# Kernel optimization log

Measured on AMD Instinct MI355X. Metric: run time of the kernel, lower is better.

## Reference

```python
import jax, jax.numpy as jnp
import numpy as np
from jax import lax

B, T, I, H = 128, 48, 128, 512


def setup_inputs() -> dict:
    key = jax.random.key(0)
    ks = jax.random.split(key, 16)
    s = lambda *sh: 1.0 / np.sqrt(sh[-1])
    inp = {
        "decoder_x": jax.random.normal(ks[0], (B, T, I), jnp.float32),
        "x": jax.random.normal(ks[1], (B, T, 3), jnp.float32),
        # xavier_normal for [num_layers=1, B, H] -> std = sqrt(2/(B+H))
        "h0": jax.random.normal(ks[2], (B, H), jnp.float32) * np.sqrt(2.0 / (B + H)),
        "W1": jax.random.normal(ks[3], (H, H), jnp.float32) * s(H),
        "b1": jnp.zeros((H,), jnp.float32),
        "W2": jax.random.normal(ks[4], (H, I), jnp.float32) * s(I),
        "b2": jnp.zeros((H,), jnp.float32),
        "W3": jax.random.normal(ks[5], (1, H), jnp.float32) * s(H),
        "b3": jnp.zeros((1,), jnp.float32),
        "W4": jax.random.normal(ks[6], (H, I + 3), jnp.float32) * s(I + 3),
        "b4": jnp.zeros((H,), jnp.float32),
        "W_ih": jax.random.normal(ks[7], (3 * H, H), jnp.float32) * s(H),
        "W_hh": jax.random.normal(ks[8], (3 * H, H), jnp.float32) * s(H),
        "b_ih": jnp.zeros((3 * H,), jnp.float32),
        "b_hh": jnp.zeros((3 * H,), jnp.float32),
        "Wfc": jax.random.normal(ks[9], (1, H), jnp.float32) * s(H),
        "bfc": jnp.zeros((1,), jnp.float32),
    }
    return inp


def reference(decoder_x, x, h0, W1, b1, W2, b2, W3, b3, W4, b4,
              W_ih, W_hh, b_ih, b_hh, Wfc, bfc):
    Bc, Tc, Ic = decoder_x.shape
    # layer2(decoder_x) is step-invariant: compute once. [B, T, H]
    w2 = jnp.einsum('bti,hi->bth', decoder_x, W2) + b2

    def step(carry, x_t):
        h, _ = carry  # h: [B, H]
        w1 = h @ W1.T + b1                              # [B, H]
        # attention energies over the T_1 encoder window
        e = jnp.tanh(w1[:, None, :] + w2) @ W3[0] + b3[0]   # [B, T]
        a = jax.nn.softmax(e, axis=1)                   # [B, T]
        c = jnp.einsum('bti,bt->bi', decoder_x, a)      # weighted context [B, I]
        y0 = jnp.concatenate([c, x_t], axis=1) @ W4.T + b4  # [B, H]
        # single-step GRU (PyTorch gate order r, z, n)
        gi = y0 @ W_ih.T + b_ih
        gh = h @ W_hh.T + b_hh
        ir, iz, in_ = jnp.split(gi, 3, axis=1)
        hr, hz, hn = jnp.split(gh, 3, axis=1)
        r = jax.nn.sigmoid(ir + hr)
        z = jax.nn.sigmoid(iz + hz)
        n = jnp.tanh(in_ + r * hn)
        h_new = (1.0 - z) * n + z * h
        return (h_new, a), None

    xs = jnp.swapaxes(x, 0, 1)  # [T, B, 3]
    (h_f, a_f), _ = lax.scan(step, (h0, jnp.zeros((Bc, Tc), decoder_x.dtype)), xs)
    re = h_f @ Wfc.T + bfc      # fc(final_output[:, -1, :])  -> [B, 1]
    return re, a_f[:, :, None]  # weighted_alpha from last step [B, T, 1]
```

## Files before the change

kernel.cpp:

```cpp
#include <hip/hip_runtime.h>


typedef _Float16 half8 __attribute__((ext_vector_type(8)));
typedef _Float16 h2v  __attribute__((ext_vector_type(2)));
typedef float    f32x4 __attribute__((ext_vector_type(4)));
typedef unsigned int u32x3 __attribute__((ext_vector_type(3)));

#define OFF_BAR   0u
#define OFF_BZ    32768u
#define OFF_BC    40960u
#define OFF_WZ    65536u
#define OFF_WCT   2162688u
#define OFF_W2H   3178496u
#define OFF_HGH   9732096u
#define OFF_ZG    9863168u
#define OFF_DW    10911744u

__device__ __forceinline__ float fexp2(float x) { return __builtin_amdgcn_exp2f(x); }
__device__ __forceinline__ float frcp(float x)  { return __builtin_amdgcn_rcpf(x); }
__device__ __forceinline__ float fast_tanh(float x) {
  x = fminf(fmaxf(x, -15.f), 15.f);
  float e = fexp2(x * 2.8853900817779268f);
  return (e - 1.f) * frcp(e + 1.f);
}
__device__ __forceinline__ float fast_sigmoid(float x) {
  x = fminf(fmaxf(x, -30.f), 30.f);
  float e = fexp2(x * 1.4426950408889634f);
  return e * frcp(e + 1.f);
}

__device__ __forceinline__ void st_f32(float* p, float v) {
  __hip_atomic_store(p, v, __ATOMIC_RELAXED, __HIP_MEMORY_SCOPE_AGENT);
}
__device__ __forceinline__ unsigned long long ld_u64(const void* p) {
  return __hip_atomic_load((const unsigned long long*)p, __ATOMIC_RELAXED,
                           __HIP_MEMORY_SCOPE_AGENT);
}
__device__ __forceinline__ void st_u32(unsigned int* p, unsigned int v) {
  __hip_atomic_store(p, v, __ATOMIC_RELAXED, __HIP_MEMORY_SCOPE_AGENT);
}
union U2 { unsigned long long u; float f[2]; };
union H4 { unsigned long long u; _Float16 h[4]; };
union HU { unsigned int u; h2v h; };

__device__ __forceinline__ void poll_ge(unsigned int* fp, bool active,
                                        unsigned int target) {
  for (;;) {
    unsigned int v = active
      ? __hip_atomic_load(fp, __ATOMIC_RELAXED, __HIP_MEMORY_SCOPE_AGENT)
      : target;
    if (__ballot(v < target) == 0) break;
    __builtin_amdgcn_s_sleep(1);
  }
  __asm__ __volatile__("" ::: "memory");
}

__global__ __launch_bounds__(256) void prep_all(
    const float* __restrict__ dx, const float* __restrict__ h0,
    const float* __restrict__ W1, const float* __restrict__ Whh,
    const float* __restrict__ b1, const float* __restrict__ bhh,
    const float* __restrict__ Wih, const float* __restrict__ W4,
    const float* __restrict__ b4, const float* __restrict__ bih,
    const float* __restrict__ W2, const float* __restrict__ b2,
    _Float16* __restrict__ hgh,
    _Float16* __restrict__ Wzh, float* __restrict__ bz,
    float* __restrict__ bc, _Float16* __restrict__ WcT,
    _Float16* __restrict__ w2h, unsigned int* __restrict__ bar)
{
  __shared__ __align__(16) char smem[58368];
  const int bid = blockIdx.x;
  const int tid = threadIdx.x;
  const int lane = tid & 63, wv = tid >> 6;

  if (bid == 0) {
    for (int i = tid; i < 8192; i += 256) bar[i] = 0u;
  } else if (bid == 1) {
    for (int n = tid; n < 2048; n += 256)
      bz[n] = (n < 512) ? b1[n] : bhh[n - 512];
  } else if (bid < 18) {
    const int o0 = (bid - 2) * 96 + wv * 24;
    for (int it = 0; it < 24; ++it) {
      const int row = o0 + it;
      const float* r = Wih + row * 512 + lane * 8;
      float s = 0.f;
#pragma unroll
      for (int u = 0; u < 8; ++u) s += r[u] * b4[lane * 8 + u];
#pragma unroll
      for (int off = 32; off >= 1; off >>= 1) s += __shfl_xor(s, off);
      if (lane == 0) bc[row] = bih[row] + s;
    }
  } else if (bid < 34) {
    const int i0 = (bid - 18) * 4096 + tid * 16;
#pragma unroll
    for (int u = 0; u < 4; ++u) {
      float4 v = *(const float4*)(h0 + i0 + u * 4);
      H4 p; p.h[0] = (_Float16)v.x; p.h[1] = (_Float16)v.y;
      p.h[2] = (_Float16)v.z; p.h[3] = (_Float16)v.w;
      *(unsigned long long*)(hgh + i0 + u * 4) = p.u;
    }
  } else if (bid < 98) {
    const int i0 = (bid - 34) * 16384 + tid * 64;
#pragma unroll 4
    for (int u = 0; u < 16; ++u) {
      const int i = i0 + u * 4;
      const float* src = (i < 262144) ? (W1 + i) : (Whh + i - 262144);
      float4 v = *(const float4*)src;
      H4 p; p.h[0] = (_Float16)v.x; p.h[1] = (_Float16)v.y;
      p.h[2] = (_Float16)v.z; p.h[3] = (_Float16)v.w;
      *(unsigned long long*)(Wzh + i) = p.u;
    }
  } else if (bid < 194) {
    float* wih = (float*)smem;
    float* w4s = (float*)(smem + 4224);
    const int o0 = (bid - 98) * 16;
    const int k = tid;
    float acc[16];
#pragma unroll
    for (int i = 0; i < 16; ++i) acc[i] = 0.f;
    for (int jc = 0; jc < 512; jc += 64) {
      __syncthreads();
      for (int idx = tid; idx < 16 * 64; idx += 256) {
        int oo = idx >> 6, jj = idx & 63;
        wih[oo * 66 + jj] = Wih[(o0 + oo) * 512 + jc + jj];
      }
      for (int idx = tid; idx < 64 * 131; idx += 256) {
        int r = idx / 131, c = idx - r * 131;
        w4s[r * 132 + c] = W4[(jc + r) * 131 + c];
      }
      __syncthreads();
      if (k < 131) {
        for (int jj = 0; jj < 64; ++jj) {
          float w4v = w4s[jj * 132 + k];
#pragma unroll
          for (int oo = 0; oo < 16; ++oo) acc[oo] += wih[oo * 66 + jj] * w4v;
        }
      }
    }
    if (k < 131) {
#pragma unroll
      for (int oo = 0; oo < 16; ++oo)
        WcT[k * 1536 + o0 + oo] = (_Float16)acc[oo];
    }
  } else {
    float* dxa = (float*)smem;
    _Float16* w2t = (_Float16*)(smem + 24576);
    const int b = bid - 194;
    for (int idx = tid; idx < 48 * 128; idx += 256)
      dxa[idx] = dx[b * 6144 + idx];
    for (int hc = 0; hc < 4; ++hc) {
      __syncthreads();
      for (int idx = tid; idx < 128 * 128; idx += 256) {
        int hl = idx >> 7, i = idx & 127;
        w2t[i * 132 + hl] = (_Float16)W2[(hc * 128 + hl) * 128 + i];
      }
      __syncthreads();
      const int hh = tid & 127;
      const int tq = tid >> 7;
      const float b2v = b2[hc * 128 + hh];
      for (int tt = tq * 24; tt < tq * 24 + 24; ++tt) {
        float acc = b2v;
#pragma unroll 4
        for (int i = 0; i < 128; ++i)
          acc += dxa[tt * 128 + i] * (float)w2t[i * 132 + hh];
        w2h[(b * 48 + tt) * 512 + hc * 128 + hh] = (_Float16)acc;
      }
    }
  }
}

__global__ __launch_bounds__(256) void prep_dw(
    const float* __restrict__ dx, const _Float16* __restrict__ WcT,
    unsigned int* __restrict__ DW12)
{
  __shared__ float dxu[16 * 128];
  const int j = blockIdx.x;
  const int tid = threadIdx.x;
  const int u0 = j * 16;
  const float4* src = (const float4*)(dx + (size_t)u0 * 128);
  float4* dst4 = (float4*)dxu;
  for (int i = tid; i < 512; i += 256) dst4[i] = src[i];
  __syncthreads();
  const int c0 = tid * 2;
  float acc[16][6];
#pragma unroll
  for (int u = 0; u < 16; ++u)
#pragma unroll
    for (int g = 0; g < 6; ++g) acc[u][g] = 0.f;
  for (int k = 0; k < 128; ++k) {
    const _Float16* wr = WcT + k * 1536 + c0;
    h2v w0 = *(const h2v*)(wr);
    h2v w1v = *(const h2v*)(wr + 512);
    h2v w2v = *(const h2v*)(wr + 1024);
    const float f0 = (float)w0[0],  f1 = (float)w0[1];
    const float f2 = (float)w1v[0], f3 = (float)w1v[1];
    const float f4 = (float)w2v[0], f5 = (float)w2v[1];
#pragma unroll
    for (int u = 0; u < 16; ++u) {
      const float d = dxu[u * 128 + k];
      acc[u][0] += d * f0; acc[u][1] += d * f1; acc[u][2] += d * f2;
      acc[u][3] += d * f3; acc[u][4] += d * f4; acc[u][5] += d * f5;
    }
  }
#pragma unroll
  for (int u = 0; u < 16; ++u) {
    unsigned int* o = DW12 + (size_t)(u0 + u) * 768 + tid * 3;
    HU p;
    p.h[0] = (_Float16)acc[u][0]; p.h[1] = (_Float16)acc[u][1]; o[0] = p.u;
    p.h[0] = (_Float16)acc[u][2]; p.h[1] = (_Float16)acc[u][3]; o[1] = p.u;
    p.h[0] = (_Float16)acc[u][4]; p.h[1] = (_Float16)acc[u][5]; o[2] = p.u;
  }
}

#define DW_STEP(TB, CUR)                                                     \
  do {                                                                       \
    _Pragma("unroll")                                                        \
    for (int j = 0; j < 4; ++j) {                                            \
      const float a = asx[(TB) * 4 + j];                                     \
      HU p0, p1, p2; p0.u = CUR[j].x; p1.u = CUR[j].y; p2.u = CUR[j].z;      \
      aR0 += a * (float)p0.h[0]; aR1 += a * (float)p0.h[1];                  \
      aZ0 += a * (float)p1.h[0]; aZ1 += a * (float)p1.h[1];                  \
      aN0 += a * (float)p2.h[0]; aN1 += a * (float)p2.h[1];                  \
    }                                                                        \
    if ((TB) < 9) {                                                          \
      _Pragma("unroll")                                                      \
      for (int j = 0; j < 4; ++j)                                            \
        CUR[j] = *(const u32x3*)(dwp + (size_t)(((TB) + 3) * 4 + j) * 768);  \
    }                                                                        \
  } while (0)

__global__ __launch_bounds__(512, 2) void decoder_main(
    const float* __restrict__ xin, const float* __restrict__ h0,
    const float* __restrict__ W3, const float* __restrict__ b3,
    const float* __restrict__ Wfc, const float* __restrict__ bfc,
    const _Float16* __restrict__ Wzh, const float* __restrict__ bz,
    const _Float16* __restrict__ WcT, const float* __restrict__ bc,
    const _Float16* __restrict__ w2h, const unsigned int* __restrict__ DW12,
    _Float16* __restrict__ hgh, float* __restrict__ zg,
    unsigned int* __restrict__ bar, float* __restrict__ out)
{
  const int tid  = threadIdx.x;
  const int lane = tid & 63;
  const int wv   = tid >> 6;
  const int bid  = blockIdx.x;
  const int grp  = bid & 7;
  const int mem  = bid >> 3;
  const int b0   = grp * 16;
  const int myrow = b0 + mem;
  const int cb   = mem * 128;
  const int myIdx = grp * 16 + mem;
  const int base16 = grp * 16;
  unsigned int* zflag = bar;
  unsigned int* hflag = bar + 4096;

  __shared__ __align__(16) _Float16 w2lds[48 * 512];
  __shared__ __align__(16) char hlds[16384];
  __shared__ __align__(16) unsigned int dwlds[24 * 768];
  __shared__ float xlds[48 * 4];
  __shared__ float wfcs[512];
  __shared__ float es[48];
  __shared__ float asx[48];
  __shared__ float red[4];

  const int m = lane & 15, q = lane >> 4;

  half8 wzf[16];
  const int ncol = cb + wv * 16 + m;
  {
    const _Float16* wrow = Wzh + ncol * 512 + q * 8;
#pragma unroll
    for (int ks = 0; ks < 16; ++ks)
      wzf[ks] = *(const half8*)(wrow + ks * 32);
  }
  const float bzv = bz[ncol];
  float w3r[8];
#pragma unroll
  for (int u = 0; u < 8; ++u) w3r[u] = W3[lane * 8 + u];
  const float b3v  = b3[0];
  const float bfcv = bfc[0];

  const int t2 = tid & 255;
  const int c0 = t2 * 2;
  const float bcR0 = bc[c0],        bcR1 = bc[c0 + 1];
  const float bcZ0 = bc[512 + c0],  bcZ1 = bc[513 + c0];
  const float bcN0 = bc[1024 + c0], bcN1 = bc[1025 + c0];
  float wxR[3][2], wxZ[3][2], wxN[3][2];
#pragma unroll
  for (int j2 = 0; j2 < 3; ++j2) {
    const _Float16* wr = WcT + (128 + j2) * 1536 + c0;
    wxR[j2][0] = (float)wr[0];    wxR[j2][1] = (float)wr[1];
    wxZ[j2][0] = (float)wr[512];  wxZ[j2][1] = (float)wr[513];
    wxN[j2][0] = (float)wr[1024]; wxN[j2][1] = (float)wr[1025];
  }
  float hA = h0[myrow * 512 + c0];
  float hB = h0[myrow * 512 + c0 + 1];

  const float* __restrict__ zrow = zg + (size_t)myrow * 2048;
  const unsigned int* __restrict__ dwp =
      DW12 + (size_t)myrow * 48 * 768 + (size_t)t2 * 3;

  {
    const half8* w2src = (const half8*)(w2h + (size_t)myrow * 48 * 512);
    half8* w2dst = (half8*)w2lds;
    for (int i = tid; i < 3072; i += 512) w2dst[i] = w2src[i];
    for (int i = tid; i < 512; i += 512) wfcs[i] = Wfc[i];
    for (int i = tid; i < 144; i += 512) {
      const int t = i / 3, j2 = i - t * 3;
      xlds[t * 4 + j2] = xin[myrow * 144 + i];
    }
    const unsigned int* dwsrc = DW12 + (size_t)myrow * 48 * 768;
    for (int i = tid; i < 24 * 256; i += 512) {
      u32x3 v = *(const u32x3*)(dwsrc + (size_t)i * 3);
      *(u32x3*)(dwlds + (size_t)i * 3) = v;
    }
  }
  __syncthreads();

  for (int step = 0; step < 48; ++step) {
    if (wv == 0)
      poll_ge(hflag + (size_t)(b0 + (lane & 15)) * 32, lane < 16,
              (unsigned int)step);
    __syncthreads();
    {
      unsigned long long hv[4];
      const char* hbase = (const char*)hgh + (size_t)b0 * 1024 + (size_t)wv * 2048;
#pragma unroll
      for (int u = 0; u < 4; ++u)
        hv[u] = ld_u64(hbase + (size_t)(u * 64 + lane) * 8);
#pragma unroll
      for (int u = 0; u < 4; ++u) {
        const int n = wv * 256 + u * 64 + lane;
        const int row = n >> 7, b8 = (n & 127) * 8;
        *(unsigned long long*)(hlds + row * 1024 + (b8 ^ ((row & 7) << 4))) = hv[u];
      }
    }
    __syncthreads();

    {
      half8 af[16];
      const char* hb = hlds + m * 1024;
      const int sw = (m & 7) << 4;
#pragma unroll
      for (int ks = 0; ks < 16; ++ks)
        af[ks] = *(const half8*)(hb + ((ks * 64 + q * 16) ^ sw));
      f32x4 acc = {bzv, bzv, bzv, bzv};
#pragma unroll
      for (int ks = 0; ks < 16; ++ks)
        acc = __builtin_amdgcn_mfma_f32_16x16x32_f16(af[ks], wzf[ks], acc, 0, 0, 0);
#pragma unroll
      for (int r = 0; r < 4; ++r)
        st_f32(&zg[(size_t)(b0 + q * 4 + r) * 2048 + ncol], acc[r]);
    }
    __syncthreads();
    if (tid == 0) st_u32(&zflag[(size_t)myIdx * 32], (unsigned int)(step + 1));

    if (wv == 0)
      poll_ge(zflag + (size_t)(base16 + (lane & 15)) * 32, lane < 16,
              (unsigned int)(step + 1));
    __syncthreads();

    float w1r[8];
#pragma unroll
    for (int u2 = 0; u2 < 4; ++u2) {
      U2 t2u; t2u.u = ld_u64(zrow + lane * 8 + u2 * 2);
      w1r[u2 * 2] = t2u.f[0]; w1r[u2 * 2 + 1] = t2u.f[1];
    }
    U2 tr, tz, tn2;
    u32x3 bA[4], bB[4], bC[4];
    if (tid < 256) {
      tr.u  = ld_u64(zrow + 512 + c0);
      tz.u  = ld_u64(zrow + 1024 + c0);
      tn2.u = ld_u64(zrow + 1536 + c0);
#pragma unroll
      for (int j = 0; j < 4; ++j) bA[j] = *(const u32x3*)(dwp + (size_t)(24 + j) * 768);
#pragma unroll
      for (int j = 0; j < 4; ++j) bB[j] = *(const u32x3*)(dwp + (size_t)(28 + j) * 768);
#pragma unroll
      for (int j = 0; j < 4; ++j) bC[j] = *(const u32x3*)(dwp + (size_t)(32 + j) * 768);
    }

    {
      for (int tt = 0; tt < 6; ++tt) {
        const int t = wv * 6 + tt;
        half8 w2v = *(const half8*)(w2lds + t * 512 + lane * 8);
        float p = 0.f;
#pragma unroll
        for (int u = 0; u < 8; ++u)
          p += w3r[u] * fast_tanh(w1r[u] + (float)w2v[u]);
#pragma unroll
        for (int off = 32; off >= 1; off >>= 1) p += __shfl_xor(p, off);
        if (lane == 0) es[t] = p + b3v;
      }
      __syncthreads();
      if (wv == 0) {
        float e = (lane < 48) ? es[lane] : -1e30f;
        float mx = e;
#pragma unroll
        for (int off = 32; off >= 1; off >>= 1) mx = fmaxf(mx, __shfl_xor(mx, off));
        float pe = (lane < 48) ? fexp2((e - mx) * 1.4426950408889634f) : 0.f;
        float s = pe;
#pragma unroll
        for (int off = 32; off >= 1; off >>= 1) s += __shfl_xor(s, off);
        float a = pe * frcp(s);
        if (lane < 48) {
          asx[lane] = a;
          if (step == 47) out[128 + myrow * 48 + lane] = a;
        }
      }
      __syncthreads();
    }

    if (tid < 256) {
      float aR0 = bcR0, aR1 = bcR1, aZ0 = bcZ0, aZ1 = bcZ1, aN0 = bcN0, aN1 = bcN1;
#pragma unroll 4
      for (int t = 0; t < 24; ++t) {
        const float a = asx[t];
        u32x3 d = *(const u32x3*)(dwlds + (size_t)(t * 256 + t2) * 3);
        HU p0, p1, p2; p0.u = d.x; p1.u = d.y; p2.u = d.z;
        aR0 += a * (float)p0.h[0]; aR1 += a * (float)p0.h[1];
        aZ0 += a * (float)p1.h[0]; aZ1 += a * (float)p1.h[1];
        aN0 += a * (float)p2.h[0]; aN1 += a * (float)p2.h[1];
      }
      DW_STEP(6, bA);  DW_STEP(7, bB);  DW_STEP(8, bC);
      DW_STEP(9, bA);  DW_STEP(10, bB); DW_STEP(11, bC);

      const float x0 = xlds[step * 4], x1 = xlds[step * 4 + 1], x2 = xlds[step * 4 + 2];
      aR0 += x0 * wxR[0][0] + x1 * wxR[1][0] + x2 * wxR[2][0];
      aR1 += x0 * wxR[0][1] + x1 * wxR[1][1] + x2 * wxR[2][1];
      aZ0 += x0 * wxZ[0][0] + x1 * wxZ[1][0] + x2 * wxZ[2][0];
      aZ1 += x0 * wxZ[0][1] + x1 * wxZ[1][1] + x2 * wxZ[2][1];
      aN0 += x0 * wxN[0][0] + x1 * wxN[1][0] + x2 * wxN[2][0];
      aN1 += x0 * wxN[0][1] + x1 * wxN[1][1] + x2 * wxN[2][1];

      const float r0 = fast_sigmoid(aR0 + tr.f[0]), r1 = fast_sigmoid(aR1 + tr.f[1]);
      const float z0 = fast_sigmoid(aZ0 + tz.f[0]), z1 = fast_sigmoid(aZ1 + tz.f[1]);
      const float n0 = fast_tanh(aN0 + r0 * tn2.f[0]), n1 = fast_tanh(aN1 + r1 * tn2.f[1]);
      hA = (1.f - z0) * n0 + z0 * hA;
      hB = (1.f - z1) * n1 + z1 * hB;
      HU hp; hp.h[0] = (_Float16)hA; hp.h[1] = (_Float16)hB;
      st_u32((unsigned int*)(hgh + myrow * 512 + c0), hp.u);
    }
    __syncthreads();
    if (tid == 0) st_u32(&hflag[(size_t)myrow * 32], (unsigned int)(step + 1));
  }

  if (tid < 256) {
    float p = hA * wfcs[c0] + hB * wfcs[c0 + 1];
#pragma unroll
    for (int off = 32; off >= 1; off >>= 1) p += __shfl_xor(p, off);
    if (lane == 0) red[wv] = p;
  }
  __syncthreads();
  if (tid == 0) out[myrow] = red[0] + red[1] + red[2] + red[3] + bfcv;
}

extern "C" void kernel_launch(void* const* d_in, const int* in_sizes, int n_in,
                              void* d_out, int out_size, void* d_ws, size_t ws_size,
                              hipStream_t stream) {
  (void)in_sizes; (void)n_in; (void)out_size; (void)ws_size;
  const float* dx  = (const float*)d_in[0];
  const float* xin = (const float*)d_in[1];
  const float* h0  = (const float*)d_in[2];
  const float* W1  = (const float*)d_in[3];
  const float* b1  = (const float*)d_in[4];
  const float* W2  = (const float*)d_in[5];
  const float* b2  = (const float*)d_in[6];
  const float* W3  = (const float*)d_in[7];
  const float* b3  = (const float*)d_in[8];
  const float* W4  = (const float*)d_in[9];
  const float* b4  = (const float*)d_in[10];
  const float* Wih = (const float*)d_in[11];
  const float* Whh = (const float*)d_in[12];
  const float* bih = (const float*)d_in[13];
  const float* bhh = (const float*)d_in[14];
  const float* Wfc = (const float*)d_in[15];
  const float* bfc = (const float*)d_in[16];

  char* ws = (char*)d_ws;
  unsigned int* bar = (unsigned int*)(ws + OFF_BAR);
  float*     bz  = (float*)(ws + OFF_BZ);
  float*     bc  = (float*)(ws + OFF_BC);
  _Float16*  Wzh = (_Float16*)(ws + OFF_WZ);
  _Float16*  WcT = (_Float16*)(ws + OFF_WCT);
  _Float16*  w2h = (_Float16*)(ws + OFF_W2H);
  _Float16*  hgh = (_Float16*)(ws + OFF_HGH);
  float*     zg  = (float*)(ws + OFF_ZG);
  unsigned int* DW12 = (unsigned int*)(ws + OFF_DW);

  prep_all<<<322, 256, 0, stream>>>(dx, h0, W1, Whh, b1, bhh, Wih, W4, b4, bih,
                                    W2, b2, hgh, Wzh, bz, bc, WcT, w2h, bar);
  prep_dw<<<384, 256, 0, stream>>>(dx, WcT, DW12);
  decoder_main<<<128, 512, 0, stream>>>(xin, h0, W3, b3, Wfc, bfc,
                                        Wzh, bz, WcT, bc, w2h, DW12,
                                        hgh, zg, bar, (float*)d_out);
}
```

Measured before the change: 846.4 us.

## Replace flag-based inter-block barriers with per-element tagged data polling

Drops the per-row flag counters and the block-wide barriers around them in the persistent decoder loop. Each published hidden-state and gate value is now a 64-bit word with the step number in the upper half and the payload in the lower half, and consumers poll the data words directly until the tag matches. This removes the flag store/poll round trips and several __syncthreads per step. In exchange it doubles the bytes moved for h and z, adds an extra zeroing pass for the tagged z buffer, and changes launch bounds to one block per SIMD set.

New measurement: 1.513 ms. +78.8%, slower.

```diff
diff --git a/kernel.cpp b/kernel.cpp
--- a/kernel.cpp
+++ b/kernel.cpp
@@ -12,9 +12,9 @@
 #define OFF_WZ    65536u
 #define OFF_WCT   2162688u
 #define OFF_W2H   3178496u
-#define OFF_HGH   9732096u
-#define OFF_ZG    9863168u
+#define OFF_HGT   9863168u
 #define OFF_DW    10911744u
+#define OFF_ZGT   29786112u
 
 __device__ __forceinline__ float fexp2(float x) { return __builtin_amdgcn_exp2f(x); }
 __device__ __forceinline__ float frcp(float x)  { return __builtin_amdgcn_rcpf(x); }
@@ -29,30 +29,22 @@
   return e * frcp(e + 1.f);
 }
 
-__device__ __forceinline__ void st_f32(float* p, float v) {
-  __hip_atomic_store(p, v, __ATOMIC_RELAXED, __HIP_MEMORY_SCOPE_AGENT);
-}
 __device__ __forceinline__ unsigned long long ld_u64(const void* p) {
   return __hip_atomic_load((const unsigned long long*)p, __ATOMIC_RELAXED,
                            __HIP_MEMORY_SCOPE_AGENT);
 }
-__device__ __forceinline__ void st_u32(unsigned int* p, unsigned int v) {
+__device__ __forceinline__ void st_u64(unsigned long long* p,
+                                       unsigned long long v) {
   __hip_atomic_store(p, v, __ATOMIC_RELAXED, __HIP_MEMORY_SCOPE_AGENT);
 }
 union U2 { unsigned long long u; float f[2]; };
 union H4 { unsigned long long u; _Float16 h[4]; };
 union HU { unsigned int u; h2v h; };
-
-__device__ __forceinline__ void poll_ge(unsigned int* fp, bool active,
-                                        unsigned int target) {
-  for (;;) {
-    unsigned int v = active
-      ? __hip_atomic_load(fp, __ATOMIC_RELAXED, __HIP_MEMORY_SCOPE_AGENT)
-      : target;
-    if (__ballot(v < target) == 0) break;
-    __builtin_amdgcn_s_sleep(1);
-  }
-  __asm__ __volatile__("" ::: "memory");
+__device__ __forceinline__ unsigned tag_of(unsigned long long v) {
+  return (unsigned)(v >> 32);
+}
+__device__ __forceinline__ float pay_f32(unsigned long long v) {
+  return __uint_as_float((unsigned)(v & 0xffffffffu));
 }
 
 __global__ __launch_bounds__(256) void prep_all(
@@ -62,10 +54,11 @@
     const float* __restrict__ Wih, const float* __restrict__ W4,
     const float* __restrict__ b4, const float* __restrict__ bih,
     const float* __restrict__ W2, const float* __restrict__ b2,
-    _Float16* __restrict__ hgh,
+    unsigned long long* __restrict__ hgt,
     _Float16* __restrict__ Wzh, float* __restrict__ bz,
     float* __restrict__ bc, _Float16* __restrict__ WcT,
-    _Float16* __restrict__ w2h, unsigned int* __restrict__ bar)
+    _Float16* __restrict__ w2h, unsigned int* __restrict__ bar,
+    unsigned long long* __restrict__ zgt)
 {
   __shared__ __align__(16) char smem[58368];
   const int bid = blockIdx.x;
@@ -90,13 +83,12 @@
       if (lane == 0) bc[row] = bih[row] + s;
     }
   } else if (bid < 34) {
-    const int i0 = (bid - 18) * 4096 + tid * 16;
-#pragma unroll
-    for (int u = 0; u < 4; ++u) {
-      float4 v = *(const float4*)(h0 + i0 + u * 4);
-      H4 p; p.h[0] = (_Float16)v.x; p.h[1] = (_Float16)v.y;
-      p.h[2] = (_Float16)v.z; p.h[3] = (_Float16)v.w;
-      *(unsigned long long*)(hgh + i0 + u * 4) = p.u;
+    const int p0 = (bid - 18) * 2048 + tid * 8;
+#pragma unroll
+    for (int u = 0; u < 8; ++u) {
+      const int p = p0 + u;
+      HU hp; hp.h[0] = (_Float16)h0[2 * p]; hp.h[1] = (_Float16)h0[2 * p + 1];
+      hgt[p] = (unsigned long long)hp.u;
     }
   } else if (bid < 98) {
     const int i0 = (bid - 34) * 16384 + tid * 64;
@@ -141,7 +133,7 @@
       for (int oo = 0; oo < 16; ++oo)
         WcT[k * 1536 + o0 + oo] = (_Float16)acc[oo];
     }
-  } else {
+  } else if (bid < 322) {
     float* dxa = (float*)smem;
     _Float16* w2t = (_Float16*)(smem + 24576);
     const int b = bid - 194;
@@ -165,6 +157,9 @@
         w2h[(b * 48 + tt) * 512 + hc * 128 + hh] = (_Float16)acc;
       }
     }
+  } else {
+    unsigned long long* z8 = zgt + (size_t)(bid - 322) * 8192;
+    for (int i = tid; i < 8192; i += 256) z8[i] = 0ull;
   }
 }
 
@@ -228,15 +223,16 @@
     }                                                                        \
   } while (0)
 
-__global__ __launch_bounds__(512, 2) void decoder_main(
+__global__ __launch_bounds__(512, 1) void decoder_main(
     const float* __restrict__ xin, const float* __restrict__ h0,
     const float* __restrict__ W3, const float* __restrict__ b3,
     const float* __restrict__ Wfc, const float* __restrict__ bfc,
     const _Float16* __restrict__ Wzh, const float* __restrict__ bz,
     const _Float16* __restrict__ WcT, const float* __restrict__ bc,
     const _Float16* __restrict__ w2h, const unsigned int* __restrict__ DW12,
-    _Float16* __restrict__ hgh, float* __restrict__ zg,
-    unsigned int* __restrict__ bar, float* __restrict__ out)
+    unsigned long long* __restrict__ hgt,
+    unsigned long long* __restrict__ zgt,
+    float* __restrict__ out)
 {
   const int tid  = threadIdx.x;
   const int lane = tid & 63;
@@ -247,10 +243,6 @@
   const int b0   = grp * 16;
   const int myrow = b0 + mem;
   const int cb   = mem * 128;
-  const int myIdx = grp * 16 + mem;
-  const int base16 = grp * 16;
-  unsigned int* zflag = bar;
-  unsigned int* hflag = bar + 4096;
 
   __shared__ __align__(16) _Float16 w2lds[48 * 512];
   __shared__ __align__(16) char hlds[16384];
@@ -294,7 +286,7 @@
   float hA = h0[myrow * 512 + c0];
   float hB = h0[myrow * 512 + c0 + 1];
 
-  const float* __restrict__ zrow = zg + (size_t)myrow * 2048;
+  const unsigned long long* __restrict__ zrow = zgt + (size_t)myrow * 2048;
   const unsigned int* __restrict__ dwp =
       DW12 + (size_t)myrow * 48 * 768 + (size_t)t2 * 3;
 
@@ -316,21 +308,31 @@
   __syncthreads();
 
   for (int step = 0; step < 48; ++step) {
-    if (wv == 0)
-      poll_ge(hflag + (size_t)(b0 + (lane & 15)) * 32, lane < 16,
-              (unsigned int)step);
-    __syncthreads();
+    const unsigned ttag  = (unsigned)step;
+    const unsigned ztag  = (unsigned)(step + 1);
+
     {
-      unsigned long long hv[4];
-      const char* hbase = (const char*)hgh + (size_t)b0 * 1024 + (size_t)wv * 2048;
-#pragma unroll
-      for (int u = 0; u < 4; ++u)
-        hv[u] = ld_u64(hbase + (size_t)(u * 64 + lane) * 8);
-#pragma unroll
-      for (int u = 0; u < 4; ++u) {
-        const int n = wv * 256 + u * 64 + lane;
-        const int row = n >> 7, b8 = (n & 127) * 8;
-        *(unsigned long long*)(hlds + row * 1024 + (b8 ^ ((row & 7) << 4))) = hv[u];
+      unsigned long long hv[8];
+      const unsigned long long* hb = hgt + (size_t)b0 * 256 + tid;
+#pragma unroll
+      for (int u = 0; u < 8; ++u) hv[u] = ld_u64(hb + u * 512);
+      for (;;) {
+        unsigned stale = 0;
+#pragma unroll
+        for (int u = 0; u < 8; ++u)
+          if (tag_of(hv[u]) < ttag) stale |= 1u << u;
+        if (__ballot(stale != 0) == 0) break;
+        __builtin_amdgcn_s_sleep(1);
+#pragma unroll
+        for (int u = 0; u < 8; ++u)
+          if (stale & (1u << u)) hv[u] = ld_u64(hb + u * 512);
+      }
+#pragma unroll
+      for (int u = 0; u < 8; ++u) {
+        const int n = tid + u * 512;
+        const int row = n >> 8, pr = n & 255;
+        *(unsigned int*)(hlds + row * 1024 + ((pr * 4) ^ ((row & 7) << 4))) =
+            (unsigned)(hv[u] & 0xffffffffu);
       }
     }
     __syncthreads();
@@ -347,29 +349,39 @@
       for (int ks = 0; ks < 16; ++ks)
         acc = __builtin_amdgcn_mfma_f32_16x16x32_f16(af[ks], wzf[ks], acc, 0, 0, 0);
 #pragma unroll
-      for (int r = 0; r < 4; ++r)
-        st_f32(&zg[(size_t)(b0 + q * 4 + r) * 2048 + ncol], acc[r]);
-    }
-    __syncthreads();
-    if (tid == 0) st_u32(&zflag[(size_t)myIdx * 32], (unsigned int)(step + 1));
-
-    if (wv == 0)
-      poll_ge(zflag + (size_t)(base16 + (lane & 15)) * 32, lane < 16,
-              (unsigned int)(step + 1));
-    __syncthreads();
+      for (int r = 0; r < 4; ++r) {
+        unsigned long long zu = ((unsigned long long)ztag << 32) |
+                                (unsigned long long)__float_as_uint(acc[r]);
+        st_u64(&zgt[(size_t)(b0 + q * 4 + r) * 2048 + ncol], zu);
+      }
+    }
 
     float w1r[8];
-#pragma unroll
-    for (int u2 = 0; u2 < 4; ++u2) {
-      U2 t2u; t2u.u = ld_u64(zrow + lane * 8 + u2 * 2);
-      w1r[u2 * 2] = t2u.f[0]; w1r[u2 * 2 + 1] = t2u.f[1];
-    }
-    U2 tr, tz, tn2;
+    {
+      unsigned long long wz[8];
+      const unsigned long long* zr8 = zrow + lane * 8;
+#pragma unroll
+      for (int k = 0; k < 8; ++k) wz[k] = ld_u64(zr8 + k);
+      for (;;) {
+        unsigned stale = 0;
+#pragma unroll
+        for (int k = 0; k < 8; ++k)
+          if (tag_of(wz[k]) < ztag) stale |= 1u << k;
+        if (__ballot(stale != 0) == 0) break;
+        __builtin_amdgcn_s_sleep(1);
+#pragma unroll
+        for (int k = 0; k < 8; ++k)
+          if (stale & (1u << k)) wz[k] = ld_u64(zr8 + k);
+      }
+#pragma unroll
+      for (int k = 0; k < 8; ++k) w1r[k] = pay_f32(wz[k]);
+    }
+    unsigned long long g[6];
     u32x3 bA[4], bB[4], bC[4];
     if (tid < 256) {
-      tr.u  = ld_u64(zrow + 512 + c0);
-      tz.u  = ld_u64(zrow + 1024 + c0);
-      tn2.u = ld_u64(zrow + 1536 + c0);
+      g[0] = ld_u64(zrow + 512 + c0);  g[1] = ld_u64(zrow + 513 + c0);
+      g[2] = ld_u64(zrow + 1024 + c0); g[3] = ld_u64(zrow + 1025 + c0);
+      g[4] = ld_u64(zrow + 1536 + c0); g[5] = ld_u64(zrow + 1537 + c0);
 #pragma unroll
       for (int j = 0; j < 4; ++j) bA[j] = *(const u32x3*)(dwp + (size_t)(24 + j) * 768);
 #pragma unroll
@@ -431,16 +443,36 @@
       aN0 += x0 * wxN[0][0] + x1 * wxN[1][0] + x2 * wxN[2][0];
       aN1 += x0 * wxN[0][1] + x1 * wxN[1][1] + x2 * wxN[2][1];
 
-      const float r0 = fast_sigmoid(aR0 + tr.f[0]), r1 = fast_sigmoid(aR1 + tr.f[1]);
-      const float z0 = fast_sigmoid(aZ0 + tz.f[0]), z1 = fast_sigmoid(aZ1 + tz.f[1]);
-      const float n0 = fast_tanh(aN0 + r0 * tn2.f[0]), n1 = fast_tanh(aN1 + r1 * tn2.f[1]);
+      {
+        const unsigned long long* ga[6] = {
+          zrow + 512 + c0,  zrow + 513 + c0,
+          zrow + 1024 + c0, zrow + 1025 + c0,
+          zrow + 1536 + c0, zrow + 1537 + c0 };
+        for (;;) {
+          unsigned stale = 0;
+#pragma unroll
+          for (int k = 0; k < 6; ++k)
+            if (tag_of(g[k]) < ztag) stale |= 1u << k;
+          if (__ballot(stale != 0) == 0) break;
+          __builtin_amdgcn_s_sleep(1);
+#pragma unroll
+          for (int k = 0; k < 6; ++k)
+            if (stale & (1u << k)) g[k] = ld_u64(ga[k]);
+        }
+      }
+      const float r0 = fast_sigmoid(aR0 + pay_f32(g[0]));
+      const float r1 = fast_sigmoid(aR1 + pay_f32(g[1]));
+      const float z0 = fast_sigmoid(aZ0 + pay_f32(g[2]));
+      const float z1 = fast_sigmoid(aZ1 + pay_f32(g[3]));
+      const float n0 = fast_tanh(aN0 + r0 * pay_f32(g[4]));
+      const float n1 = fast_tanh(aN1 + r1 * pay_f32(g[5]));
       hA = (1.f - z0) * n0 + z0 * hA;
       hB = (1.f - z1) * n1 + z1 * hB;
       HU hp; hp.h[0] = (_Float16)hA; hp.h[1] = (_Float16)hB;
-      st_u32((unsigned int*)(hgh + myrow * 512 + c0), hp.u);
-    }
-    __syncthreads();
-    if (tid == 0) st_u32(&hflag[(size_t)myrow * 32], (unsigned int)(step + 1));
+      unsigned long long hu = ((unsigned long long)(step + 1) << 32) |
+                              (unsigned long long)hp.u;
+      st_u64(&hgt[(size_t)myrow * 256 + t2], hu);
+    }
   }
 
   if (tid < 256) {
@@ -482,14 +514,14 @@
   _Float16*  Wzh = (_Float16*)(ws + OFF_WZ);
   _Float16*  WcT = (_Float16*)(ws + OFF_WCT);
   _Float16*  w2h = (_Float16*)(ws + OFF_W2H);
-  _Float16*  hgh = (_Float16*)(ws + OFF_HGH);
-  float*     zg  = (float*)(ws + OFF_ZG);
+  unsigned long long* hgt = (unsigned long long*)(ws + OFF_HGT);
+  unsigned long long* zgt = (unsigned long long*)(ws + OFF_ZGT);
   unsigned int* DW12 = (unsigned int*)(ws + OFF_DW);
 
-  prep_all<<<322, 256, 0, stream>>>(dx, h0, W1, Whh, b1, bhh, Wih, W4, b4, bih,
-                                    W2, b2, hgh, Wzh, bz, bc, WcT, w2h, bar);
+  prep_all<<<354, 256, 0, stream>>>(dx, h0, W1, Whh, b1, bhh, Wih, W4, b4, bih,
+                                    W2, b2, hgt, Wzh, bz, bc, WcT, w2h, bar, zgt);
   prep_dw<<<384, 256, 0, stream>>>(dx, WcT, DW12);
   decoder_main<<<128, 512, 0, stream>>>(xin, h0, W3, b3, Wfc, bfc,
                                         Wzh, bz, WcT, bc, w2h, DW12,
-                                        hgh, zg, bar, (float*)d_out);
-}
+                                        hgt, zgt, (float*)d_out);
+}
```

## Coalesce inter-block h and z exchanges into 16-byte cache-bypassing vector transfers

Applied to the files above, without the earlier changes.

Inter-block exchanges of the hidden state and the gate pre-activations switch from many scalar relaxed atomic loads and stores to 16-byte global loads and stores with sc0 sc1 cache-bypass bits, written in inline asm. MFMA results and new h values are first staged in new LDS tiles so each is written with one coalesced store, and the z row is read once into LDS for all consumers. Explicit vmcnt drains are added before the flags are published. The extra LDS lowers the launch bound to one block per CU, and Wfc is now read directly from global memory.

Result: no change. 853.2 us (+0.8%).

```diff
diff --git a/kernel.cpp b/kernel.cpp
--- a/kernel.cpp
+++ b/kernel.cpp
@@ -29,19 +29,34 @@
   return e * frcp(e + 1.f);
 }
 
-__device__ __forceinline__ void st_f32(float* p, float v) {
-  __hip_atomic_store(p, v, __ATOMIC_RELAXED, __HIP_MEMORY_SCOPE_AGENT);
-}
-__device__ __forceinline__ unsigned long long ld_u64(const void* p) {
-  return __hip_atomic_load((const unsigned long long*)p, __ATOMIC_RELAXED,
-                           __HIP_MEMORY_SCOPE_AGENT);
-}
 __device__ __forceinline__ void st_u32(unsigned int* p, unsigned int v) {
   __hip_atomic_store(p, v, __ATOMIC_RELAXED, __HIP_MEMORY_SCOPE_AGENT);
 }
-union U2 { unsigned long long u; float f[2]; };
 union H4 { unsigned long long u; _Float16 h[4]; };
 union HU { unsigned int u; h2v h; };
+
+__device__ __forceinline__ f32x4 ld16_sc(const void* p) {
+  f32x4 v;
+  asm volatile("global_load_dwordx4 %0, %1, off sc0 sc1\n\t"
+               "s_waitcnt vmcnt(0)"
+               : "=v"(v) : "v"(p) : "memory");
+  return v;
+}
+__device__ __forceinline__ void ld16x2_sc(const void* p0, const void* p1,
+                                          f32x4* a, f32x4* b) {
+  asm volatile("global_load_dwordx4 %0, %2, off sc0 sc1\n\t"
+               "global_load_dwordx4 %1, %3, off sc0 sc1\n\t"
+               "s_waitcnt vmcnt(0)"
+               : "=v"(*a), "=v"(*b) : "v"(p0), "v"(p1) : "memory");
+}
+__device__ __forceinline__ void st16_sc(void* p, f32x4 v) {
+  asm volatile("global_store_dwordx4 %0, %1, off sc0 sc1"
+               :: "v"(p), "v"(v) : "memory");
+}
+__device__ __forceinline__ void drain_vm() {
+  asm volatile("s_waitcnt vmcnt(0)" ::: "memory");
+  __builtin_amdgcn_sched_barrier(0);
+}
 
 __device__ __forceinline__ void poll_ge(unsigned int* fp, bool active,
                                         unsigned int target) {
@@ -228,7 +243,7 @@
     }                                                                        \
   } while (0)
 
-__global__ __launch_bounds__(512, 2) void decoder_main(
+__global__ __launch_bounds__(512, 1) void decoder_main(
     const float* __restrict__ xin, const float* __restrict__ h0,
     const float* __restrict__ W3, const float* __restrict__ b3,
     const float* __restrict__ Wfc, const float* __restrict__ bfc,
@@ -255,8 +270,10 @@
   __shared__ __align__(16) _Float16 w2lds[48 * 512];
   __shared__ __align__(16) char hlds[16384];
   __shared__ __align__(16) unsigned int dwlds[24 * 768];
+  __shared__ __align__(16) float ztile[16 * 132];
+  __shared__ __align__(16) float zrowlds[2048];
+  __shared__ __align__(16) unsigned int hpack[256];
   __shared__ float xlds[48 * 4];
-  __shared__ float wfcs[512];
   __shared__ float es[48];
   __shared__ float asx[48];
   __shared__ float red[4];
@@ -302,7 +319,6 @@
     const half8* w2src = (const half8*)(w2h + (size_t)myrow * 48 * 512);
     half8* w2dst = (half8*)w2lds;
     for (int i = tid; i < 3072; i += 512) w2dst[i] = w2src[i];
-    for (int i = tid; i < 512; i += 512) wfcs[i] = Wfc[i];
     for (int i = tid; i < 144; i += 512) {
       const int t = i / 3, j2 = i - t * 3;
       xlds[t * 4 + j2] = xin[myrow * 144 + i];
@@ -321,17 +337,14 @@
               (unsigned int)step);
     __syncthreads();
     {
-      unsigned long long hv[4];
-      const char* hbase = (const char*)hgh + (size_t)b0 * 1024 + (size_t)wv * 2048;
-#pragma unroll
-      for (int u = 0; u < 4; ++u)
-        hv[u] = ld_u64(hbase + (size_t)(u * 64 + lane) * 8);
-#pragma unroll
-      for (int u = 0; u < 4; ++u) {
-        const int n = wv * 256 + u * 64 + lane;
-        const int row = n >> 7, b8 = (n & 127) * 8;
-        *(unsigned long long*)(hlds + row * 1024 + (b8 ^ ((row & 7) << 4))) = hv[u];
-      }
+      const char* hb = (const char*)hgh + (size_t)b0 * 1024 + (size_t)tid * 16;
+      f32x4 hv0, hv1;
+      ld16x2_sc(hb, hb + 8192, &hv0, &hv1);
+      const int n0 = tid, n1 = tid + 512;
+      const int r0 = n0 >> 6, j0 = n0 & 63;
+      const int r1 = n1 >> 6, j1 = n1 & 63;
+      *(f32x4*)(hlds + r0 * 1024 + ((j0 * 16) ^ ((r0 & 7) << 4))) = hv0;
+      *(f32x4*)(hlds + r1 * 1024 + ((j1 * 16) ^ ((r1 & 7) << 4))) = hv1;
     }
     __syncthreads();
 
@@ -348,8 +361,15 @@
         acc = __builtin_amdgcn_mfma_f32_16x16x32_f16(af[ks], wzf[ks], acc, 0, 0, 0);
 #pragma unroll
       for (int r = 0; r < 4; ++r)
-        st_f32(&zg[(size_t)(b0 + q * 4 + r) * 2048 + ncol], acc[r]);
-    }
+        ztile[(q * 4 + r) * 132 + wv * 16 + m] = acc[r];
+    }
+    __syncthreads();
+    {
+      const int zr = tid >> 5, cq = tid & 31;
+      f32x4 zv = *(const f32x4*)(ztile + zr * 132 + cq * 4);
+      st16_sc(zg + (size_t)(b0 + zr) * 2048 + cb + cq * 4, zv);
+    }
+    drain_vm();
     __syncthreads();
     if (tid == 0) st_u32(&zflag[(size_t)myIdx * 32], (unsigned int)(step + 1));
 
@@ -357,19 +377,14 @@
       poll_ge(zflag + (size_t)(base16 + (lane & 15)) * 32, lane < 16,
               (unsigned int)(step + 1));
     __syncthreads();
-
-    float w1r[8];
-#pragma unroll
-    for (int u2 = 0; u2 < 4; ++u2) {
-      U2 t2u; t2u.u = ld_u64(zrow + lane * 8 + u2 * 2);
-      w1r[u2 * 2] = t2u.f[0]; w1r[u2 * 2 + 1] = t2u.f[1];
-    }
-    U2 tr, tz, tn2;
+    {
+      f32x4 zv = ld16_sc((const char*)zrow + (size_t)tid * 16);
+      *(f32x4*)(zrowlds + tid * 4) = zv;
+    }
+    __syncthreads();
+
     u32x3 bA[4], bB[4], bC[4];
     if (tid < 256) {
-      tr.u  = ld_u64(zrow + 512 + c0);
-      tz.u  = ld_u64(zrow + 1024 + c0);
-      tn2.u = ld_u64(zrow + 1536 + c0);
 #pragma unroll
       for (int j = 0; j < 4; ++j) bA[j] = *(const u32x3*)(dwp + (size_t)(24 + j) * 768);
 #pragma unroll
@@ -379,6 +394,9 @@
     }
 
     {
+      float w1r[8];
+#pragma unroll
+      for (int u = 0; u < 8; ++u) w1r[u] = zrowlds[lane * 8 + u];
       for (int tt = 0; tt < 6; ++tt) {
         const int t = wv * 6 + tt;
         half8 w2v = *(const half8*)(w2lds + t * 512 + lane * 8);
@@ -431,20 +449,28 @@
       aN0 += x0 * wxN[0][0] + x1 * wxN[1][0] + x2 * wxN[2][0];
       aN1 += x0 * wxN[0][1] + x1 * wxN[1][1] + x2 * wxN[2][1];
 
-      const float r0 = fast_sigmoid(aR0 + tr.f[0]), r1 = fast_sigmoid(aR1 + tr.f[1]);
-      const float z0 = fast_sigmoid(aZ0 + tz.f[0]), z1 = fast_sigmoid(aZ1 + tz.f[1]);
-      const float n0 = fast_tanh(aN0 + r0 * tn2.f[0]), n1 = fast_tanh(aN1 + r1 * tn2.f[1]);
+      const float2 gR = *(const float2*)(zrowlds + 512 + c0);
+      const float2 gZ = *(const float2*)(zrowlds + 1024 + c0);
+      const float2 gN = *(const float2*)(zrowlds + 1536 + c0);
+      const float r0 = fast_sigmoid(aR0 + gR.x), r1 = fast_sigmoid(aR1 + gR.y);
+      const float z0 = fast_sigmoid(aZ0 + gZ.x), z1 = fast_sigmoid(aZ1 + gZ.y);
+      const float n0 = fast_tanh(aN0 + r0 * gN.x), n1 = fast_tanh(aN1 + r1 * gN.y);
       hA = (1.f - z0) * n0 + z0 * hA;
       hB = (1.f - z1) * n1 + z1 * hB;
       HU hp; hp.h[0] = (_Float16)hA; hp.h[1] = (_Float16)hB;
-      st_u32((unsigned int*)(hgh + myrow * 512 + c0), hp.u);
-    }
-    __syncthreads();
+      hpack[t2] = hp.u;
+    }
+    __syncthreads();
+    if (tid < 64) {
+      f32x4 hv = *(const f32x4*)((const char*)hpack + tid * 16);
+      st16_sc((char*)hgh + (size_t)myrow * 1024 + (size_t)tid * 16, hv);
+    }
+    drain_vm();
     if (tid == 0) st_u32(&hflag[(size_t)myrow * 32], (unsigned int)(step + 1));
   }
 
   if (tid < 256) {
-    float p = hA * wfcs[c0] + hB * wfcs[c0 + 1];
+    float p = hA * Wfc[c0] + hB * Wfc[c0 + 1];
 #pragma unroll
     for (int off = 32; off >= 1; off >>= 1) p += __shfl_xor(p, off);
     if (lane == 0) red[wv] = p;
```
